# Kernel tuning notes

Hardware: AMD Instinct MI355X
Metric: run time of the kernel (lower is better)

## Reference

```python
import jax, jax.numpy as jnp
import numpy as np

D_MODEL = 1024
D_HIDDEN = 1024  # must equal D_MODEL (SSM adds C(h) [.,d_model] + D(x) [.,d_hidden])
B, T = 8, 1022   # T chosen so T+2 == D_MODEL, required by the `x @ x_res` batched matmul


def setup_inputs() -> dict:
    key = jax.random.key(0)
    ks = jax.random.split(key, 12)
    def w(k, shape, s=0.02):
        return jax.random.normal(k, shape, jnp.float32) * s
    return {
        "x": jax.random.normal(ks[0], (B, T, D_MODEL), jnp.float32),
        "w1": w(ks[1], (D_MODEL, D_MODEL)),
        "w2": w(ks[2], (D_MODEL, D_MODEL)),
        "w_last": w(ks[3], (D_MODEL, D_MODEL)),
        "conv_w": w(ks[4], (D_MODEL, 1, 3), 0.1),  # depthwise conv kernel [out, in/groups, k]
        "conv_b": jnp.zeros((D_MODEL,), jnp.float32),
        "A": jnp.abs(jax.random.normal(ks[5], (D_HIDDEN,), jnp.float32)) + 0.1,  # positive -> stable decay
        "wB": w(ks[6], (D_MODEL, D_HIDDEN)), "bB": jnp.zeros((D_HIDDEN,), jnp.float32),
        "wC": w(ks[7], (D_HIDDEN, D_MODEL)), "bC": jnp.zeros((D_MODEL,), jnp.float32),
        "wD": w(ks[8], (D_MODEL, D_HIDDEN)), "bD": jnp.zeros((D_HIDDEN,), jnp.float32),
        "wdelta": w(ks[9], (D_MODEL, D_HIDDEN)), "bdelta": jnp.zeros((D_HIDDEN,), jnp.float32),
    }


def _scan_combine(l, r):
    # linear recurrence h_t = a_t * h_{t-1} + b_t as an associative op
    aL, bL = l
    aR, bR = r
    return (aL * aR, aR * bL + bR)


def reference(x, w1, w2, w_last, conv_w, conv_b, A, wB, bB, wC, bC, wD, bD, wdelta, bdelta):
    x = x @ w1  # [B,T,D]
    # depthwise causal-ish conv, padding=2 on both sides (as in torch code) -> length T+2
    xc = jnp.transpose(x, (0, 2, 1))  # [B,D,T]
    xc = jax.lax.conv_general_dilated(
        xc, conv_w, window_strides=(1,), padding=[(2, 2)],
        dimension_numbers=("NCH", "OIH", "NCH"), feature_group_count=D_MODEL)
    xc = xc + conv_b[None, :, None]
    x = jnp.transpose(xc, (0, 2, 1))  # [B, T+2, D]
    x = jax.nn.silu(x)
    # --- SSM selective scan ---
    x_delta = jax.nn.softplus(x @ wdelta + bdelta)      # [B,T+2,Dh]
    A_bar = jnp.exp(-x_delta * A)                       # [B,T+2,Dh]
    B_x = x @ wB + bB                                   # [B,T+2,Dh]
    _, h = jax.lax.associative_scan(_scan_combine, (A_bar, B_x), axis=1)
    ssm_out = (h @ wC + bC) + (x @ wD + bD)             # [B,T+2,D] (Dh == D)
    # --- gating + output ---
    x_res = jax.nn.silu(ssm_out @ w2)                   # [B,T+2,D]
    z = jnp.matmul(ssm_out, x_res)                      # batched matmul: valid since D == T+2
    out = z @ w_last                                    # [B, T+2, D]
    return out
```

## Files before the change

### kernel.cpp

```cpp
#include <hip/hip_runtime.h>

typedef __bf16 bf16x8 __attribute__((ext_vector_type(8)));
typedef float  f32x4  __attribute__((ext_vector_type(4)));
typedef unsigned short u16x8 __attribute__((ext_vector_type(8)));

__device__ __forceinline__ float b2f(unsigned short u) {
  union { float f; unsigned int i; } v; v.i = ((unsigned int)u) << 16; return v.f;
}
__device__ __forceinline__ unsigned short f2b(float f) {
  union { float f; unsigned int i; } v; v.f = f;
  unsigned int r = v.i + 0x7fffu + ((v.i >> 16) & 1u);
  return (unsigned short)(r >> 16);
}

__device__ __forceinline__ void async_copy16(const unsigned short* g, unsigned short* l) {
  __builtin_amdgcn_global_load_lds(
      (__attribute__((address_space(1))) void*)g,
      (__attribute__((address_space(3))) void*)l, 16, 0, 0);
}

__global__ void k_prep_w(const float* w0, const float* w1_, const float* w2_,
                         const float* w3_, const float* w4_, const float* w5_,
                         const float* w6_, unsigned short* dst) {
  const float* srcs[7] = {w0, w1_, w2_, w3_, w4_, w5_, w6_};
  const float* src = srcs[blockIdx.z];
  unsigned short* d = dst + ((size_t)blockIdx.z << 20);
  __shared__ float tile[32][33];
  const int bn = blockIdx.x << 5, bk = blockIdx.y << 5;
  const int tx = threadIdx.x, ty = threadIdx.y;
#pragma unroll
  for (int i = 0; i < 4; ++i)
    tile[ty + i * 8][tx] = src[(size_t)(bk + ty + i * 8) * 1024 + bn + tx];
  __syncthreads();
#pragma unroll
  for (int i = 0; i < 4; ++i)
    d[(size_t)(bn + ty + i * 8) * 1024 + bk + tx] = f2b(tile[tx][ty + i * 8]);
}

__global__ void k_prep_cw(const float* __restrict__ cw, float* __restrict__ cwT) {
  const int idx = blockIdx.x * 256 + threadIdx.x;
  const int d = idx & 1023, j = idx >> 10;
  cwT[idx] = cw[d * 3 + j];
}

__global__ void k_cast_x(const float* __restrict__ x, unsigned short* __restrict__ xb) {
  const size_t i = ((size_t)blockIdx.x * 256 + threadIdx.x) << 2;
  const int d = (int)(i & 1023);
  const int row = (int)(i >> 10);
  const int t = row & 1023, b = row >> 10;
  float4 v = make_float4(0.f, 0.f, 0.f, 0.f);
  if (t < 1022) v = *(const float4*)&x[((size_t)(b * 1022 + t) << 10) + d];
  ushort4 o;
  o.x = f2b(v.x); o.y = f2b(v.y); o.z = f2b(v.z); o.w = f2b(v.w);
  *(ushort4*)&xb[i] = o;
}

__global__ void k_conv_silu(const unsigned short* __restrict__ x1, const float* __restrict__ cwT,
                            const float* __restrict__ cb, unsigned short* __restrict__ xs) {
  const int gid = blockIdx.x * 256 + threadIdx.x;
  const int row = gid >> 7;
  const int d0 = (gid & 127) << 3;
  const int b = row >> 10, i = row & 1023;
  float acc[8];
  {
    float4 c0 = *(const float4*)&cb[d0], c1 = *(const float4*)&cb[d0 + 4];
    acc[0] = c0.x; acc[1] = c0.y; acc[2] = c0.z; acc[3] = c0.w;
    acc[4] = c1.x; acc[5] = c1.y; acc[6] = c1.z; acc[7] = c1.w;
  }
#pragma unroll
  for (int j = 0; j < 3; ++j) {
    const int t = i + j - 2;
    if (t >= 0) {
      u16x8 v = *(const u16x8*)&x1[((size_t)(b * 1024 + t) << 10) + d0];
      float4 w0 = *(const float4*)&cwT[j * 1024 + d0];
      float4 w1 = *(const float4*)&cwT[j * 1024 + d0 + 4];
      acc[0] += b2f(v[0]) * w0.x; acc[1] += b2f(v[1]) * w0.y;
      acc[2] += b2f(v[2]) * w0.z; acc[3] += b2f(v[3]) * w0.w;
      acc[4] += b2f(v[4]) * w1.x; acc[5] += b2f(v[5]) * w1.y;
      acc[6] += b2f(v[6]) * w1.z; acc[7] += b2f(v[7]) * w1.w;
    }
  }
  u16x8 o;
#pragma unroll
  for (int k = 0; k < 8; ++k) {
    float s = acc[k] / (1.f + __expf(-acc[k]));
    o[k] = f2b(s);
  }
  *(u16x8*)&xs[((size_t)row << 10) + d0] = o;
}

__global__ void k_scan1(const float* __restrict__ Abar, const unsigned short* __restrict__ Bx,
                        float* __restrict__ cA, float* __restrict__ cB) {
  const int g = blockIdx.x * 256 + threadIdx.x;
  const int d = g & 1023, bc = g >> 10;
  const int b = bc >> 4, c = bc & 15;
  size_t base = ((size_t)(b * 1024 + c * 64) << 10) + d;
  float aA = 1.f, aB = 0.f;
  for (int t = 0; t < 64; ++t) {
    float a = Abar[base], bx = b2f(Bx[base]);
    aA *= a; aB = a * aB + bx; base += 1024;
  }
  cA[g] = aA; cB[g] = aB;
}
__global__ void k_scan2(const float* __restrict__ cA, const float* __restrict__ cB,
                        float* __restrict__ carry) {
  const int g = blockIdx.x * 256 + threadIdx.x;
  const int d = g & 1023, b = g >> 10;
  float a[16], bb[16];
#pragma unroll
  for (int c = 0; c < 16; ++c) {
    const int idx = ((b * 16 + c) << 10) + d;
    a[c] = cA[idx]; bb[c] = cB[idx];
  }
  float sB = 0.f;
#pragma unroll
  for (int c = 0; c < 16; ++c) {
    carry[((b * 16 + c) << 10) + d] = sB;
    sB = a[c] * sB + bb[c];
  }
}
__global__ void k_scan3(const float* __restrict__ Abar, const unsigned short* __restrict__ Bx,
                        const float* __restrict__ carry, unsigned short* __restrict__ hb) {
  const int g = blockIdx.x * 256 + threadIdx.x;
  const int d = g & 1023, bc = g >> 10;
  const int b = bc >> 4, c = bc & 15;
  size_t base = ((size_t)(b * 1024 + c * 64) << 10) + d;
  float h = carry[g];
  for (int t = 0; t < 64; ++t) {
    float a = Abar[base], bx = b2f(Bx[base]);
    h = a * h + bx;
    hb[base] = f2b(h);
    base += 1024;
  }
}

__global__ void k_transpose_xres(const unsigned short* __restrict__ src,
                                 unsigned short* __restrict__ dst) {
  __shared__ unsigned short tile[32][33];
  const int b = blockIdx.z;
  const int bx = blockIdx.x << 5, by = blockIdx.y << 5;
  const int tx = threadIdx.x, ty = threadIdx.y;
  const unsigned short* s = src + ((size_t)b << 20);
  unsigned short* d = dst + ((size_t)b << 20);
#pragma unroll
  for (int i = 0; i < 4; ++i)
    tile[ty + i * 8][tx] = s[(size_t)(by + ty + i * 8) * 1024 + bx + tx];
  __syncthreads();
#pragma unroll
  for (int i = 0; i < 4; ++i)
    d[(size_t)(bx + ty + i * 8) * 1024 + by + tx] = tile[tx][ty + i * 8];
}

template <int EPI, bool BATCHB>
__global__ __launch_bounds__(256)
void k_gemm(const unsigned short* __restrict__ A, const unsigned short* __restrict__ Bt,
            void* __restrict__ outp, const float* __restrict__ aux1,
            const void* __restrict__ aux2) {
  __shared__ unsigned short As[2][128 * 64];
  __shared__ unsigned short Bs[2][128 * 64];
  const int tid = threadIdx.x;

  const int nxb = gridDim.x;
  const int nwg = nxb * gridDim.y;
  int lin = blockIdx.y * nxb + blockIdx.x;
  lin = (lin & 7) * (nwg >> 3) + (lin >> 3);
  const int CH = nxb << 3;
  const int grp = lin / CH, idx = lin % CH;
  const int m0 = ((grp << 3) + (idx & 7)) << 7;
  const int n0 = (idx >> 3) << 7;

  const int wid = tid >> 6, l = tid & 63;
  const int wr = ((wid >> 1) << 6);
  const int wc = ((wid & 1) << 6);
  const int lr = l & 15, kg = l >> 4;
  const unsigned short* Bp = BATCHB ? Bt + ((size_t)(m0 >> 10) << 20) : Bt;

  f32x4 acc[4][4];
#pragma unroll
  for (int i = 0; i < 4; ++i)
#pragma unroll
    for (int j = 0; j < 4; ++j) acc[i][j] = (f32x4){0.f, 0.f, 0.f, 0.f};

  const int frow = tid >> 3;
  const int fchunk = (tid & 7) ^ (frow & 7);
  const unsigned short* ga[4];
  const unsigned short* gb[4];
#pragma unroll
  for (int it = 0; it < 4; ++it) {
    ga[it] = A  + (size_t)(m0 + frow + it * 32) * 1024 + (fchunk << 3);
    gb[it] = Bp + (size_t)(n0 + frow + it * 32) * 1024 + (fchunk << 3);
  }

#define STAGE(buf)                                                              \
  {                                                                             \
    _Pragma("unroll")                                                           \
    for (int it = 0; it < 4; ++it)                                              \
      async_copy16(ga[it], &As[buf][(tid << 3) + it * 2048]);                   \
    _Pragma("unroll")                                                           \
    for (int it = 0; it < 4; ++it)                                              \
      async_copy16(gb[it], &Bs[buf][(tid << 3) + it * 2048]);                   \
    _Pragma("unroll")                                                           \
    for (int it = 0; it < 4; ++it) { ga[it] += 64; gb[it] += 64; }              \
  }

  const int c0 = kg ^ (lr & 7);
  const int aOff0 = ((wr + lr) << 7) + (c0 << 4);
  const int aOff1 = aOff0 ^ 64;
  const int bOff0 = ((wc + lr) << 7) + (c0 << 4);
  const int bOff1 = bOff0 ^ 64;
  const char* AsB = (const char*)&As[0][0];
  const char* BsB = (const char*)&Bs[0][0];

  STAGE(0);
  STAGE(1);

#pragma unroll
  for (int t = 0; t < 16; ++t) {
    const int cur = t & 1;
    if (t < 15) asm volatile("s_waitcnt vmcnt(8)" ::: "memory");
    else        asm volatile("s_waitcnt vmcnt(0)" ::: "memory");
    __builtin_amdgcn_s_barrier();
    __builtin_amdgcn_sched_barrier(0);
    __builtin_amdgcn_s_setprio(1);
    const char* pa = AsB + (cur << 14);
    const char* pb = BsB + (cur << 14);
    {
      bf16x8 aF[4], bF[4];
#pragma unroll
      for (int mi = 0; mi < 4; ++mi) aF[mi] = *(const bf16x8*)(pa + aOff0 + mi * 2048);
#pragma unroll
      for (int ni = 0; ni < 4; ++ni) bF[ni] = *(const bf16x8*)(pb + bOff0 + ni * 2048);
#pragma unroll
      for (int mi = 0; mi < 4; ++mi)
#pragma unroll
        for (int ni = 0; ni < 4; ++ni)
          acc[mi][ni] = __builtin_amdgcn_mfma_f32_16x16x32_bf16(bF[ni], aF[mi], acc[mi][ni], 0, 0, 0);
    }
    {
      bf16x8 aF[4], bF[4];
#pragma unroll
      for (int mi = 0; mi < 4; ++mi) aF[mi] = *(const bf16x8*)(pa + aOff1 + mi * 2048);
#pragma unroll
      for (int ni = 0; ni < 4; ++ni) bF[ni] = *(const bf16x8*)(pb + bOff1 + ni * 2048);
#pragma unroll
      for (int mi = 0; mi < 4; ++mi)
#pragma unroll
        for (int ni = 0; ni < 4; ++ni)
          acc[mi][ni] = __builtin_amdgcn_mfma_f32_16x16x32_bf16(bF[ni], aF[mi], acc[mi][ni], 0, 0, 0);
    }
    __builtin_amdgcn_s_setprio(0);
    asm volatile("s_waitcnt lgkmcnt(0)" ::: "memory");
    __builtin_amdgcn_s_barrier();
    __builtin_amdgcn_sched_barrier(0);
    if (t + 2 < 16) STAGE(cur);
  }
#undef STAGE

#pragma unroll
  for (int mi = 0; mi < 4; ++mi) {
    const int row = m0 + wr + mi * 16 + lr;
    const size_t rbase = (size_t)row << 10;
#pragma unroll
    for (int ni = 0; ni < 4; ++ni) {
      const int colb = n0 + wc + ni * 16 + (kg << 2);
      const f32x4 v = acc[mi][ni];
      if (EPI == 0) {
        ushort4 o; o.x = f2b(v[0]); o.y = f2b(v[1]); o.z = f2b(v[2]); o.w = f2b(v[3]);
        *(ushort4*)&((unsigned short*)outp)[rbase + colb] = o;
      } else if (EPI == 1) {
        const float4 b4 = *(const float4*)&aux1[colb];
        const float4 a4 = *(const float4*)&((const float*)aux2)[colb];
        float4 o;
        {
          float t0 = v[0] + b4.x; float sp = (t0 > 15.f) ? t0 : __logf(1.f + __expf(t0));
          o.x = __expf(-sp * a4.x);
          float t1 = v[1] + b4.y; sp = (t1 > 15.f) ? t1 : __logf(1.f + __expf(t1));
          o.y = __expf(-sp * a4.y);
          float t2 = v[2] + b4.z; sp = (t2 > 15.f) ? t2 : __logf(1.f + __expf(t2));
          o.z = __expf(-sp * a4.z);
          float t3 = v[3] + b4.w; sp = (t3 > 15.f) ? t3 : __logf(1.f + __expf(t3));
          o.w = __expf(-sp * a4.w);
        }
        *(float4*)&((float*)outp)[rbase + colb] = o;
      } else if (EPI == 2) {
        const float4 b4 = *(const float4*)&aux1[colb];
        ushort4 o;
        o.x = f2b(v[0] + b4.x); o.y = f2b(v[1] + b4.y);
        o.z = f2b(v[2] + b4.z); o.w = f2b(v[3] + b4.w);
        *(ushort4*)&((unsigned short*)outp)[rbase + colb] = o;
      } else if (EPI == 3) {
        const float4 b4 = *(const float4*)&aux1[colb];
        const ushort4 xv = *(const ushort4*)&((const unsigned short*)aux2)[rbase + colb];
        ushort4 o;
        o.x = f2b(v[0] + b4.x + b2f(xv.x)); o.y = f2b(v[1] + b4.y + b2f(xv.y));
        o.z = f2b(v[2] + b4.z + b2f(xv.z)); o.w = f2b(v[3] + b4.w + b2f(xv.w));
        *(ushort4*)&((unsigned short*)outp)[rbase + colb] = o;
      } else if (EPI == 4) {
        ushort4 o;
        o.x = f2b(v[0] / (1.f + __expf(-v[0]))); o.y = f2b(v[1] / (1.f + __expf(-v[1])));
        o.z = f2b(v[2] / (1.f + __expf(-v[2]))); o.w = f2b(v[3] / (1.f + __expf(-v[3])));
        *(ushort4*)&((unsigned short*)outp)[rbase + colb] = o;
      } else {
        float4 o; o.x = v[0]; o.y = v[1]; o.z = v[2]; o.w = v[3];
        *(float4*)&((float*)outp)[rbase + colb] = o;
      }
    }
  }
}

extern "C" void kernel_launch(void* const* d_in, const int* in_sizes, int n_in,
                              void* d_out, int out_size, void* d_ws, size_t ws_size,
                              hipStream_t stream) {
  const float* x      = (const float*)d_in[0];
  const float* w1     = (const float*)d_in[1];
  const float* w2     = (const float*)d_in[2];
  const float* w_last = (const float*)d_in[3];
  const float* conv_w = (const float*)d_in[4];
  const float* conv_b = (const float*)d_in[5];
  const float* Avec   = (const float*)d_in[6];
  const float* wB     = (const float*)d_in[7];
  const float* bB     = (const float*)d_in[8];
  const float* wC     = (const float*)d_in[9];
  const float* bC     = (const float*)d_in[10];
  const float* wD     = (const float*)d_in[11];
  const float* bD     = (const float*)d_in[12];
  const float* wdelta = (const float*)d_in[13];
  const float* bdelta = (const float*)d_in[14];

  char* ws = (char*)d_ws;
  const size_t MB = 1ull << 20;
  const size_t NW = 1ull << 20;
  unsigned short* wT   = (unsigned short*)(ws);
  unsigned short* xb   = (unsigned short*)(ws + 14 * MB);
  unsigned short* x1   = (unsigned short*)(ws + 30 * MB);
  unsigned short* xs   = (unsigned short*)(ws + 46 * MB);
  float*          Abar = (float*)(ws + 62 * MB);
  unsigned short* Bx   = (unsigned short*)(ws + 94 * MB);
  unsigned short* xD   = (unsigned short*)(ws + 110 * MB);
  float*          cA   = (float*)(ws + 126 * MB);
  float*          cB   = (float*)(ws + 126 * MB + 512 * 1024);
  float*          carry= (float*)(ws + 127 * MB);
  float*          cwT  = (float*)(ws + 127 * MB + 512 * 1024);
  unsigned short* hb    = xs;
  unsigned short* ssm   = xb;
  unsigned short* xres  = x1;
  unsigned short* xresT = (unsigned short*)(ws + 62 * MB);
  unsigned short* z     = (unsigned short*)(ws + 78 * MB);

  dim3 bT(32, 8);
  dim3 gG(8, 64);

  k_prep_w<<<dim3(32, 32, 7), bT, 0, stream>>>(w1, wdelta, wB, wD, wC, w2, w_last, wT);
  k_prep_cw<<<12, 256, 0, stream>>>(conv_w, cwT);
  k_cast_x<<<8192, 256, 0, stream>>>(x, xb);
  k_gemm<0, false><<<gG, 256, 0, stream>>>(xb, wT + 0 * NW, x1, nullptr, nullptr);
  k_conv_silu<<<4096, 256, 0, stream>>>(x1, cwT, conv_b, xs);
  k_gemm<1, false><<<gG, 256, 0, stream>>>(xs, wT + 1 * NW, Abar, bdelta, (const void*)Avec);
  k_gemm<2, false><<<gG, 256, 0, stream>>>(xs, wT + 2 * NW, Bx, bB, nullptr);
  k_gemm<2, false><<<gG, 256, 0, stream>>>(xs, wT + 3 * NW, xD, bD, nullptr);
  k_scan1<<<512, 256, 0, stream>>>(Abar, Bx, cA, cB);
  k_scan2<<<32, 256, 0, stream>>>(cA, cB, carry);
  k_scan3<<<512, 256, 0, stream>>>(Abar, Bx, carry, hb);
  k_gemm<3, false><<<gG, 256, 0, stream>>>(hb, wT + 4 * NW, ssm, bC, (const void*)xD);
  k_gemm<4, false><<<gG, 256, 0, stream>>>(ssm, wT + 5 * NW, xres, nullptr, nullptr);
  k_transpose_xres<<<dim3(32, 32, 8), bT, 0, stream>>>(xres, xresT);
  k_gemm<0, true><<<gG, 256, 0, stream>>>(ssm, xresT, z, nullptr, nullptr);
  k_gemm<5, false><<<gG, 256, 0, stream>>>(z, wT + 6 * NW, (float*)d_out, nullptr, nullptr);
}
```

Baseline: 254.4 us.

## Restructure GEMM to 128x256 tiles, 8 waves, triple-buffered interleaved loads

The GEMM kernel now uses 512-thread blocks computing 128x256 output tiles with 8 waves, and a three-stage LDS ring in place of double buffering. Global-to-LDS copies for the next stage are split into three pieces and interleaved with four MFMA phases per K step, so loads overlap compute at a finer grain. The block swizzle is simplified to a fixed mapping for the 4x64 grid. This adds more barriers per iteration and a larger LDS footprint (about 144KB), and it hardcodes the grid shape.

```diff
diff --git a/kernel.cpp b/kernel.cpp
--- a/kernel.cpp
+++ b/kernel.cpp
@@ -152,26 +152,22 @@
 }
 
 template <int EPI, bool BATCHB>
-__global__ __launch_bounds__(256)
+__global__ __launch_bounds__(512, 2)
 void k_gemm(const unsigned short* __restrict__ A, const unsigned short* __restrict__ Bt,
             void* __restrict__ outp, const float* __restrict__ aux1,
             const void* __restrict__ aux2) {
-  __shared__ unsigned short As[2][128 * 64];
-  __shared__ unsigned short Bs[2][128 * 64];
+  __shared__ unsigned short As[3 * 8192];
+  __shared__ unsigned short Bs[3 * 16384];
   const int tid = threadIdx.x;
 
-  const int nxb = gridDim.x;
-  const int nwg = nxb * gridDim.y;
-  int lin = blockIdx.y * nxb + blockIdx.x;
-  lin = (lin & 7) * (nwg >> 3) + (lin >> 3);
-  const int CH = nxb << 3;
-  const int grp = lin / CH, idx = lin % CH;
-  const int m0 = ((grp << 3) + (idx & 7)) << 7;
-  const int n0 = (idx >> 3) << 7;
+  const int lin = blockIdx.y * gridDim.x + blockIdx.x;
+  const int sw = (lin & 7) * 32 + (lin >> 3);
+  const int m0 = (sw & 63) << 7;
+  const int n0 = (sw >> 6) << 8;
 
   const int wid = tid >> 6, l = tid & 63;
-  const int wr = ((wid >> 1) << 6);
-  const int wc = ((wid & 1) << 6);
+  const int wr = (wid >> 2) << 6;
+  const int wc = (wid & 3) << 6;
   const int lr = l & 15, kg = l >> 4;
   const unsigned short* Bp = BATCHB ? Bt + ((size_t)(m0 >> 10) << 20) : Bt;
 
@@ -183,78 +179,118 @@
 
   const int frow = tid >> 3;
   const int fchunk = (tid & 7) ^ (frow & 7);
-  const unsigned short* ga[4];
-  const unsigned short* gb[4];
-#pragma unroll
-  for (int it = 0; it < 4; ++it) {
-    ga[it] = A  + (size_t)(m0 + frow + it * 32) * 1024 + (fchunk << 3);
-    gb[it] = Bp + (size_t)(n0 + frow + it * 32) * 1024 + (fchunk << 3);
-  }
-
-#define STAGE(buf)                                                              \
-  {                                                                             \
-    _Pragma("unroll")                                                           \
-    for (int it = 0; it < 4; ++it)                                              \
-      async_copy16(ga[it], &As[buf][(tid << 3) + it * 2048]);                   \
-    _Pragma("unroll")                                                           \
-    for (int it = 0; it < 4; ++it)                                              \
-      async_copy16(gb[it], &Bs[buf][(tid << 3) + it * 2048]);                   \
-    _Pragma("unroll")                                                           \
-    for (int it = 0; it < 4; ++it) { ga[it] += 64; gb[it] += 64; }              \
-  }
-
-  const int c0 = kg ^ (lr & 7);
-  const int aOff0 = ((wr + lr) << 7) + (c0 << 4);
-  const int aOff1 = aOff0 ^ 64;
-  const int bOff0 = ((wc + lr) << 7) + (c0 << 4);
-  const int bOff1 = bOff0 ^ 64;
-  const char* AsB = (const char*)&As[0][0];
-  const char* BsB = (const char*)&Bs[0][0];
-
-  STAGE(0);
-  STAGE(1);
+  const unsigned short* ga0 = A  + (size_t)(m0 + frow) * 1024 + (fchunk << 3);
+  const unsigned short* ga1 = ga0 + 64 * 1024;
+  const unsigned short* gb0 = Bp + (size_t)(n0 + frow) * 1024 + (fchunk << 3);
+  const unsigned short* gb1 = gb0 + 64 * 1024;
+  const unsigned short* gb2 = gb0 + 128 * 1024;
+  const unsigned short* gb3 = gb0 + 192 * 1024;
+
+#define STAGE_A(buf)  { async_copy16(ga0, &As[(buf) * 8192 + tid * 8]);                 \
+                        async_copy16(ga1, &As[(buf) * 8192 + 4096 + tid * 8]); }
+#define STAGE_B01(buf){ async_copy16(gb0, &Bs[(buf) * 16384 + tid * 8]);                \
+                        async_copy16(gb1, &Bs[(buf) * 16384 + 4096 + tid * 8]); }
+#define STAGE_B23(buf){ async_copy16(gb2, &Bs[(buf) * 16384 + 8192 + tid * 8]);         \
+                        async_copy16(gb3, &Bs[(buf) * 16384 + 12288 + tid * 8]); }
+#define ADVANCE()     { ga0 += 64; ga1 += 64; gb0 += 64; gb1 += 64; gb2 += 64; gb3 += 64; }
+
+  const int cc0 = (kg ^ (lr & 7)) << 4;
+  const int cc1 = cc0 ^ 64;
+  int rowA[4], rowB[4];
+#pragma unroll
+  for (int i = 0; i < 4; ++i) {
+    rowA[i] = (wr + i * 16 + lr) << 7;
+    rowB[i] = (wc + i * 16 + lr) << 7;
+  }
+  const char* AsB = (const char*)&As[0];
+  const char* BsB = (const char*)&Bs[0];
+
+  STAGE_A(0); STAGE_B01(0); STAGE_B23(0); ADVANCE();
+  STAGE_A(1); STAGE_B01(1); STAGE_B23(1); ADVANCE();
 
 #pragma unroll
   for (int t = 0; t < 16; ++t) {
-    const int cur = t & 1;
-    if (t < 15) asm volatile("s_waitcnt vmcnt(8)" ::: "memory");
+    const int cur = t % 3;
+    const int ib = (t + 2) % 3;
+    if (t < 15) asm volatile("s_waitcnt vmcnt(6)" ::: "memory");
     else        asm volatile("s_waitcnt vmcnt(0)" ::: "memory");
     __builtin_amdgcn_s_barrier();
+
+    const char* pa = AsB + cur * 16384;
+    const char* pb = BsB + cur * 32768;
+    bf16x8 aF[4], bF[4];
+
+#pragma unroll
+    for (int mi = 0; mi < 4; ++mi) aF[mi] = *(const bf16x8*)(pa + rowA[mi] + cc0);
+    bF[0] = *(const bf16x8*)(pb + rowB[0] + cc0);
+    bF[1] = *(const bf16x8*)(pb + rowB[1] + cc0);
+    if (t < 14) STAGE_A(ib);
+    __builtin_amdgcn_sched_barrier(0);
+    __builtin_amdgcn_s_barrier();
+    asm volatile("s_waitcnt lgkmcnt(0)" ::: "memory");
     __builtin_amdgcn_sched_barrier(0);
     __builtin_amdgcn_s_setprio(1);
-    const char* pa = AsB + (cur << 14);
-    const char* pb = BsB + (cur << 14);
-    {
-      bf16x8 aF[4], bF[4];
-#pragma unroll
-      for (int mi = 0; mi < 4; ++mi) aF[mi] = *(const bf16x8*)(pa + aOff0 + mi * 2048);
-#pragma unroll
-      for (int ni = 0; ni < 4; ++ni) bF[ni] = *(const bf16x8*)(pb + bOff0 + ni * 2048);
-#pragma unroll
-      for (int mi = 0; mi < 4; ++mi)
-#pragma unroll
-        for (int ni = 0; ni < 4; ++ni)
-          acc[mi][ni] = __builtin_amdgcn_mfma_f32_16x16x32_bf16(bF[ni], aF[mi], acc[mi][ni], 0, 0, 0);
-    }
-    {
-      bf16x8 aF[4], bF[4];
-#pragma unroll
-      for (int mi = 0; mi < 4; ++mi) aF[mi] = *(const bf16x8*)(pa + aOff1 + mi * 2048);
-#pragma unroll
-      for (int ni = 0; ni < 4; ++ni) bF[ni] = *(const bf16x8*)(pb + bOff1 + ni * 2048);
-#pragma unroll
-      for (int mi = 0; mi < 4; ++mi)
-#pragma unroll
-        for (int ni = 0; ni < 4; ++ni)
-          acc[mi][ni] = __builtin_amdgcn_mfma_f32_16x16x32_bf16(bF[ni], aF[mi], acc[mi][ni], 0, 0, 0);
+#pragma unroll
+    for (int mi = 0; mi < 4; ++mi) {
+      acc[mi][0] = __builtin_amdgcn_mfma_f32_16x16x32_bf16(bF[0], aF[mi], acc[mi][0], 0, 0, 0);
+      acc[mi][1] = __builtin_amdgcn_mfma_f32_16x16x32_bf16(bF[1], aF[mi], acc[mi][1], 0, 0, 0);
     }
     __builtin_amdgcn_s_setprio(0);
+    __builtin_amdgcn_s_barrier();
+
+    bF[2] = *(const bf16x8*)(pb + rowB[2] + cc0);
+    bF[3] = *(const bf16x8*)(pb + rowB[3] + cc0);
+    if (t < 14) STAGE_B01(ib);
+    __builtin_amdgcn_sched_barrier(0);
+    __builtin_amdgcn_s_barrier();
     asm volatile("s_waitcnt lgkmcnt(0)" ::: "memory");
-    __builtin_amdgcn_s_barrier();
-    __builtin_amdgcn_sched_barrier(0);
-    if (t + 2 < 16) STAGE(cur);
-  }
-#undef STAGE
+    __builtin_amdgcn_sched_barrier(0);
+    __builtin_amdgcn_s_setprio(1);
+#pragma unroll
+    for (int mi = 0; mi < 4; ++mi) {
+      acc[mi][2] = __builtin_amdgcn_mfma_f32_16x16x32_bf16(bF[2], aF[mi], acc[mi][2], 0, 0, 0);
+      acc[mi][3] = __builtin_amdgcn_mfma_f32_16x16x32_bf16(bF[3], aF[mi], acc[mi][3], 0, 0, 0);
+    }
+    __builtin_amdgcn_s_setprio(0);
+    __builtin_amdgcn_s_barrier();
+
+#pragma unroll
+    for (int mi = 0; mi < 4; ++mi) aF[mi] = *(const bf16x8*)(pa + rowA[mi] + cc1);
+    bF[0] = *(const bf16x8*)(pb + rowB[0] + cc1);
+    bF[1] = *(const bf16x8*)(pb + rowB[1] + cc1);
+    if (t < 14) { STAGE_B23(ib); ADVANCE(); }
+    __builtin_amdgcn_sched_barrier(0);
+    __builtin_amdgcn_s_barrier();
+    asm volatile("s_waitcnt lgkmcnt(0)" ::: "memory");
+    __builtin_amdgcn_sched_barrier(0);
+    __builtin_amdgcn_s_setprio(1);
+#pragma unroll
+    for (int mi = 0; mi < 4; ++mi) {
+      acc[mi][0] = __builtin_amdgcn_mfma_f32_16x16x32_bf16(bF[0], aF[mi], acc[mi][0], 0, 0, 0);
+      acc[mi][1] = __builtin_amdgcn_mfma_f32_16x16x32_bf16(bF[1], aF[mi], acc[mi][1], 0, 0, 0);
+    }
+    __builtin_amdgcn_s_setprio(0);
+    __builtin_amdgcn_s_barrier();
+
+    bF[2] = *(const bf16x8*)(pb + rowB[2] + cc1);
+    bF[3] = *(const bf16x8*)(pb + rowB[3] + cc1);
+    __builtin_amdgcn_sched_barrier(0);
+    __builtin_amdgcn_s_barrier();
+    asm volatile("s_waitcnt lgkmcnt(0)" ::: "memory");
+    __builtin_amdgcn_sched_barrier(0);
+    __builtin_amdgcn_s_setprio(1);
+#pragma unroll
+    for (int mi = 0; mi < 4; ++mi) {
+      acc[mi][2] = __builtin_amdgcn_mfma_f32_16x16x32_bf16(bF[2], aF[mi], acc[mi][2], 0, 0, 0);
+      acc[mi][3] = __builtin_amdgcn_mfma_f32_16x16x32_bf16(bF[3], aF[mi], acc[mi][3], 0, 0, 0);
+    }
+    __builtin_amdgcn_s_setprio(0);
+    __builtin_amdgcn_s_barrier();
+  }
+#undef STAGE_A
+#undef STAGE_B01
+#undef STAGE_B23
+#undef ADVANCE
 
 #pragma unroll
   for (int mi = 0; mi < 4; ++mi) {
@@ -348,22 +384,22 @@
   unsigned short* z     = (unsigned short*)(ws + 78 * MB);
 
   dim3 bT(32, 8);
-  dim3 gG(8, 64);
+  dim3 gG(4, 64);
 
   k_prep_w<<<dim3(32, 32, 7), bT, 0, stream>>>(w1, wdelta, wB, wD, wC, w2, w_last, wT);
   k_prep_cw<<<12, 256, 0, stream>>>(conv_w, cwT);
   k_cast_x<<<8192, 256, 0, stream>>>(x, xb);
-  k_gemm<0, false><<<gG, 256, 0, stream>>>(xb, wT + 0 * NW, x1, nullptr, nullptr);
+  k_gemm<0, false><<<gG, 512, 0, stream>>>(xb, wT + 0 * NW, x1, nullptr, nullptr);
   k_conv_silu<<<4096, 256, 0, stream>>>(x1, cwT, conv_b, xs);
-  k_gemm<1, false><<<gG, 256, 0, stream>>>(xs, wT + 1 * NW, Abar, bdelta, (const void*)Avec);
-  k_gemm<2, false><<<gG, 256, 0, stream>>>(xs, wT + 2 * NW, Bx, bB, nullptr);
-  k_gemm<2, false><<<gG, 256, 0, stream>>>(xs, wT + 3 * NW, xD, bD, nullptr);
+  k_gemm<1, false><<<gG, 512, 0, stream>>>(xs, wT + 1 * NW, Abar, bdelta, (const void*)Avec);
+  k_gemm<2, false><<<gG, 512, 0, stream>>>(xs, wT + 2 * NW, Bx, bB, nullptr);
+  k_gemm<2, false><<<gG, 512, 0, stream>>>(xs, wT + 3 * NW, xD, bD, nullptr);
   k_scan1<<<512, 256, 0, stream>>>(Abar, Bx, cA, cB);
   k_scan2<<<32, 256, 0, stream>>>(cA, cB, carry);
   k_scan3<<<512, 256, 0, stream>>>(Abar, Bx, carry, hb);
-  k_gemm<3, false><<<gG, 256, 0, stream>>>(hb, wT + 4 * NW, ssm, bC, (const void*)xD);
-  k_gemm<4, false><<<gG, 256, 0, stream>>>(ssm, wT + 5 * NW, xres, nullptr, nullptr);
+  k_gemm<3, false><<<gG, 512, 0, stream>>>(hb, wT + 4 * NW, ssm, bC, (const void*)xD);
+  k_gemm<4, false><<<gG, 512, 0, stream>>>(ssm, wT + 5 * NW, xres, nullptr, nullptr);
   k_transpose_xres<<<dim3(32, 32, 8), bT, 0, stream>>>(xres, xresT);
-  k_gemm<0, true><<<gG, 256, 0, stream>>>(ssm, xresT, z, nullptr, nullptr);
-  k_gemm<5, false><<<gG, 256, 0, stream>>>(z, wT + 6 * NW, (float*)d_out, nullptr, nullptr);
-}
+  k_gemm<0, true><<<gG, 512, 0, stream>>>(ssm, xresT, z, nullptr, nullptr);
+  k_gemm<5, false><<<gG, 512, 0, stream>>>(z, wT + 6 * NW, (float*)d_out, nullptr, nullptr);
+}
```

Measured after the change: 292.0 us. 14.8% more time.
